# Kernel optimization log

Measured on AMD Instinct MI355X. Metric: run time of the kernel, lower is better.

## Reference

```python
import jax, jax.numpy as jnp
import numpy as np
import math

B = 16384; IN_DIM = 512; OUT_DIM = 256
D_MODEL = 512; N_HEADS = 8; E_LAYERS = 3; D_FF = 2048
FACTOR = 5; EPS = 1e-5
E_HEAD = D_MODEL // N_HEADS


def setup_inputs() -> dict:
    key = jax.random.key(0)
    ks = jax.random.split(key, 16)
    def w(k, shape):
        return jax.random.normal(k, shape, dtype=jnp.float32) * 0.02
    return {
        "x": jax.random.normal(ks[0], (B, IN_DIM), dtype=jnp.float32),
        "w_in": w(ks[1], (IN_DIM, D_MODEL)), "b_in": jnp.zeros((D_MODEL,), jnp.float32),
        "wq": w(ks[2], (D_MODEL, D_MODEL)), "bq": jnp.zeros((D_MODEL,), jnp.float32),
        "wk": w(ks[3], (D_MODEL, D_MODEL)), "bk": jnp.zeros((D_MODEL,), jnp.float32),
        "wv": w(ks[4], (D_MODEL, D_MODEL)), "bv": jnp.zeros((D_MODEL,), jnp.float32),
        "wo": w(ks[5], (D_MODEL, D_MODEL)), "bo": jnp.zeros((D_MODEL,), jnp.float32),
        "conv1_w": w(ks[6], (E_LAYERS, D_MODEL, D_FF)), "conv1_b": jnp.zeros((E_LAYERS, D_FF), jnp.float32),
        "conv2_w": w(ks[7], (E_LAYERS, D_FF, D_MODEL)), "conv2_b": jnp.zeros((E_LAYERS, D_MODEL), jnp.float32),
        "n1_g": jnp.ones((E_LAYERS, D_MODEL), jnp.float32), "n1_b": jnp.zeros((E_LAYERS, D_MODEL), jnp.float32),
        "n2_g": jnp.ones((E_LAYERS, D_MODEL), jnp.float32), "n2_b": jnp.zeros((E_LAYERS, D_MODEL), jnp.float32),
        "norm_g": jnp.ones((D_MODEL,), jnp.float32), "norm_b": jnp.zeros((D_MODEL,), jnp.float32),
        "w1": w(ks[8], (D_MODEL, D_FF)), "b1": jnp.zeros((D_FF,), jnp.float32),
        "w2": w(ks[9], (D_FF, OUT_DIM)), "b2": jnp.zeros((OUT_DIM,), jnp.float32),
    }


def _layernorm(x, g, b):
    m = jnp.mean(x, axis=-1, keepdims=True)
    v = jnp.mean(jnp.square(x - m), axis=-1, keepdims=True)
    return (x - m) * jax.lax.rsqrt(v + EPS) * g + b


def _prob_attention(q, k, v):
    # q,k,v: [B,H,L,E]; Informer ProbAttention with mask_flag=False.
    Bq, H, L, Eh = q.shape
    L_K = k.shape[2]
    # static (Python-level) sparse-attention sizes, as in the source
    U_part = min(L_K, max(1, FACTOR * int(np.ceil(np.log(max(L_K, 1.1))))))
    u = min(L, max(1, FACTOR * int(np.ceil(np.log(max(L, 1.1))))))
    step = L_K // max(1, U_part)
    idx = jnp.arange(0, L_K, step)                      # deterministic key sample
    k_s = k[:, :, idx, :]                               # [B,H,S,E] (no L_Q expand needed)
    qk_s = jnp.einsum('bhle,bhse->bhls', q, k_s)        # sampled QK scores
    M = qk_s.max(-1) - qk_s.sum(-1) / L_K               # sparsity measure [B,H,L]
    _, top = jax.lax.top_k(M, u)                        # top-u query indices [B,H,u]
    q_r = jnp.take_along_axis(q, top[..., None], axis=2)  # gather Q_reduce [B,H,u,E]
    scale = 1.0 / math.sqrt(Eh)
    scores = jnp.einsum('bhue,bhke->bhuk', q_r, k) * scale
    attn = jax.nn.softmax(scores, axis=-1)
    upd = jnp.einsum('bhuk,bhkd->bhud', attn, v)        # [B,H,u,D]
    # initial context = mean of V (mask_flag=False), then scatter top-u rows
    ctx = jnp.broadcast_to(v.mean(axis=2, keepdims=True), (Bq, H, L, v.shape[-1]))
    bi = jnp.arange(Bq)[:, None, None]
    hi = jnp.arange(H)[None, :, None]
    return ctx.at[bi, hi, top].set(upd)


def _attention_layer(x, wq, bq, wk, bk, wv, bv, wo, bo):
    Bx, L, _ = x.shape
    def proj(w, b):
        return (x @ w + b).reshape(Bx, L, N_HEADS, E_HEAD).transpose(0, 2, 1, 3)
    ctx = _prob_attention(proj(wq, bq), proj(wk, bk), proj(wv, bv))
    ctx = ctx.transpose(0, 2, 1, 3).reshape(Bx, L, -1)
    return ctx @ wo + bo


def _forward(x, w_in, b_in, wq, bq, wk, bk, wv, bv, wo, bo,
             conv1_w, conv1_b, conv2_w, conv2_b,
             n1_g, n1_b, n2_g, n2_b, norm_g, norm_b, w1, b1, w2, b2):
    h = (x @ w_in + b_in)[:, None, :]  # [B, 1, d_model] -- seq_len hardwired to 1
    for i in range(E_LAYERS):
        # NOTE: attention projection weights are SHARED across layers (as in source)
        a = _attention_layer(h, wq, bq, wk, bk, wv, bv, wo, bo)
        h = _layernorm(h + a, n1_g[i], n1_b[i])
        y = jax.nn.gelu(h @ conv1_w[i] + conv1_b[i], approximate=False)  # 1x1 conv == linear
        y = y @ conv2_w[i] + conv2_b[i]
        h = _layernorm(h + y, n2_g[i], n2_b[i])
    h = _layernorm(h, norm_g, norm_b)[:, 0, :]
    o = jax.nn.gelu(h @ w1 + b1, approximate=False)
    return o @ w2 + b2


def reference(x, w_in, b_in, wq, bq, wk, bk, wv, bv, wo, bo,
              conv1_w, conv1_b, conv2_w, conv2_b,
              n1_g, n1_b, n2_g, n2_b, norm_g, norm_b, w1, b1, w2, b2):
    return _forward(x, w_in, b_in, wq, bq, wk, bk, wv, bv, wo, bo,
                    conv1_w, conv1_b, conv2_w, conv2_b,
                    n1_g, n1_b, n2_g, n2_b, norm_g, norm_b, w1, b1, w2, b2)
```

## Files before the change

kernel.cpp:

```cpp
#include <hip/hip_runtime.h>
#include <hip/hip_bf16.h>
#include <math.h>

#define B_ROWS 16384
#define DM 512
#define DFF 2048
#define DOUT 256
#define EPSV 1e-5f

typedef __hip_bfloat16 bf16;
typedef __attribute__((ext_vector_type(8))) short short8;
typedef __attribute__((ext_vector_type(4))) float f32x4;

__device__ __forceinline__ float gelu_f(float x) {
    return 0.5f * x * (1.0f + erff(x * 0.70710678118654752f));
}

__device__ __forceinline__ void gload16(const void* g, void* l) {
    __builtin_amdgcn_global_load_lds((const __attribute__((address_space(1))) void*)g,
                                     (__attribute__((address_space(3))) void*)l, 16, 0, 0);
}

template<bool GELU, bool OUTF, bool OUTB>
__global__ __launch_bounds__(256, 2)
void gemm_kernel(const bf16* __restrict__ A, const bf16* __restrict__ BT,
                 const float* __restrict__ bias,
                 float* __restrict__ Cf, bf16* __restrict__ Cb,
                 int M, int N, int K)
{
    __shared__ __align__(16) bf16 lA[128 * 32];
    __shared__ __align__(16) bf16 lB[128 * 32];

    const int t    = threadIdx.x;
    const int lane = t & 63;
    const int w    = t >> 6;
    const int wr   = w >> 1, wc = w & 1;
    const int fr   = lane & 15, kg = lane >> 4;
    const long bm = (long)blockIdx.y * 128;
    const long bn = (long)blockIdx.x * 128;

    const int lr = t >> 2;
    const int lc = (t & 3) * 8;

    const bf16* Ag0 = A + (bm + lr) * (long)K + lc;
    const bf16* Ag1 = Ag0 + 64L * K;
    const bf16* Bg0 = BT + (bn + lr) * (long)K + lc;
    const bf16* Bg1 = Bg0 + 64L * K;

    bf16* lAd0 = lA + t * 8;
    bf16* lAd1 = lAd0 + 2048;
    bf16* lBd0 = lB + t * 8;
    bf16* lBd1 = lBd0 + 2048;

    f32x4 acc[4][4];
#pragma unroll
    for (int i = 0; i < 4; i++)
#pragma unroll
        for (int j = 0; j < 4; j++) acc[i][j] = (f32x4){0.f, 0.f, 0.f, 0.f};

    const int nk = K >> 5;
    for (int kt = 0; kt < nk; ++kt) {
        gload16(Ag0, lAd0);
        gload16(Ag1, lAd1);
        gload16(Bg0, lBd0);
        gload16(Bg1, lBd1);
        Ag0 += 32; Ag1 += 32; Bg0 += 32; Bg1 += 32;
        __syncthreads();

        short8 af[4], bv[4];
#pragma unroll
        for (int m = 0; m < 4; m++)
            af[m] = *(const short8*)(lA + (wr * 64 + m * 16 + fr) * 32 + kg * 8);
#pragma unroll
        for (int n = 0; n < 4; n++)
            bv[n] = *(const short8*)(lB + (wc * 64 + n * 16 + fr) * 32 + kg * 8);
#pragma unroll
        for (int m = 0; m < 4; m++)
#pragma unroll
            for (int n = 0; n < 4; n++)
                acc[m][n] = __builtin_amdgcn_mfma_f32_16x16x32_bf16(af[m], bv[n], acc[m][n], 0, 0, 0);
        __syncthreads();
    }

#pragma unroll
    for (int m = 0; m < 4; m++) {
        const long row0 = bm + wr * 64 + m * 16 + kg * 4;
#pragma unroll
        for (int n = 0; n < 4; n++) {
            const long col = bn + wc * 64 + n * 16 + fr;
            const float bias_v = bias ? bias[col] : 0.0f;
#pragma unroll
            for (int r = 0; r < 4; r++) {
                float v = acc[m][n][r] + bias_v;
                if (GELU) v = gelu_f(v);
                const long idx = (row0 + r) * (long)N + col;
                if (OUTF) Cf[idx] = v;
                if (OUTB) Cb[idx] = __float2bfloat16(v);
            }
        }
    }
}

__global__ __launch_bounds__(256)
void ln_kernel(const float* __restrict__ x, const float* __restrict__ add,
               const float* __restrict__ g, const float* __restrict__ bb,
               float* __restrict__ outf, bf16* __restrict__ outb)
{
    const int w    = threadIdx.x >> 6;
    const int lane = threadIdx.x & 63;
    const long row = (long)blockIdx.x * 4 + w;
    const int c0   = lane * 8;

    const float* xr = x + row * DM + c0;
    float4 a0 = *(const float4*)xr;
    float4 a1 = *(const float4*)(xr + 4);
    float v[8] = {a0.x, a0.y, a0.z, a0.w, a1.x, a1.y, a1.z, a1.w};
    if (add) {
        const float* ar = add + row * DM + c0;
        float4 d0 = *(const float4*)ar;
        float4 d1 = *(const float4*)(ar + 4);
        v[0] += d0.x; v[1] += d0.y; v[2] += d0.z; v[3] += d0.w;
        v[4] += d1.x; v[5] += d1.y; v[6] += d1.z; v[7] += d1.w;
    }
    float s = 0.f;
#pragma unroll
    for (int j = 0; j < 8; j++) s += v[j];
#pragma unroll
    for (int off = 32; off > 0; off >>= 1) s += __shfl_xor(s, off);
    const float mean = s * (1.0f / 512.0f);

    float q = 0.f;
#pragma unroll
    for (int j = 0; j < 8; j++) { v[j] -= mean; q += v[j] * v[j]; }
#pragma unroll
    for (int off = 32; off > 0; off >>= 1) q += __shfl_xor(q, off);
    const float rstd = rsqrtf(q * (1.0f / 512.0f) + EPSV);

    float4 g0 = *(const float4*)(g + c0);
    float4 g1 = *(const float4*)(g + c0 + 4);
    float4 b0 = *(const float4*)(bb + c0);
    float4 b1 = *(const float4*)(bb + c0 + 4);
    float y[8];
    y[0] = v[0] * rstd * g0.x + b0.x; y[1] = v[1] * rstd * g0.y + b0.y;
    y[2] = v[2] * rstd * g0.z + b0.z; y[3] = v[3] * rstd * g0.w + b0.w;
    y[4] = v[4] * rstd * g1.x + b1.x; y[5] = v[5] * rstd * g1.y + b1.y;
    y[6] = v[6] * rstd * g1.z + b1.z; y[7] = v[7] * rstd * g1.w + b1.w;

    if (outf) {
        float* orow = outf + row * DM + c0;
        *(float4*)orow       = make_float4(y[0], y[1], y[2], y[3]);
        *(float4*)(orow + 4) = make_float4(y[4], y[5], y[6], y[7]);
    }
    if (outb) {
        bf16 tmpb[8];
#pragma unroll
        for (int j = 0; j < 8; j++) tmpb[j] = __float2bfloat16(y[j]);
        *(uint4*)(outb + row * DM + c0) = *(const uint4*)tmpb;
    }
}

__global__ __launch_bounds__(256)
void transpose_bf16_kernel(const float* __restrict__ src, bf16* __restrict__ dst, int K, int N)
{
    __shared__ float tile[32][33];
    const long boff = (long)blockIdx.z * K * N;
    src += boff; dst += boff;
    const int n0 = blockIdx.x * 32, k0 = blockIdx.y * 32;
    const int tx = threadIdx.x & 31, ty = threadIdx.x >> 5;
#pragma unroll
    for (int j = 0; j < 32; j += 8)
        tile[ty + j][tx] = src[(long)(k0 + ty + j) * N + n0 + tx];
    __syncthreads();
#pragma unroll
    for (int j = 0; j < 32; j += 8)
        dst[(long)(n0 + ty + j) * K + k0 + tx] = __float2bfloat16(tile[tx][ty + j]);
}

__global__ __launch_bounds__(256)
void cvt_kernel(const float* __restrict__ src, bf16* __restrict__ dst, long n4)
{
    const long i = (long)blockIdx.x * 256 + threadIdx.x;
    if (i >= n4) return;
    const float4 vv = *(const float4*)(src + i * 4);
    bf16 t[4] = {__float2bfloat16(vv.x), __float2bfloat16(vv.y),
                 __float2bfloat16(vv.z), __float2bfloat16(vv.w)};
    *(uint2*)(dst + i * 4) = *(const uint2*)t;
}

__global__ __launch_bounds__(256)
void ba_kernel(const float* __restrict__ bv, const float* __restrict__ wo,
               const float* __restrict__ bo, float* __restrict__ ba)
{
    const int n = blockIdx.x * 256 + threadIdx.x;
    float s = bo[n];
    for (int j = 0; j < DM; j++) s += bv[j] * wo[(long)j * DM + n];
    ba[n] = s;
}

extern "C" void kernel_launch(void* const* d_in, const int* in_sizes, int n_in,
                              void* d_out, int out_size, void* d_ws, size_t ws_size,
                              hipStream_t stream)
{
    const float* x       = (const float*)d_in[0];
    const float* w_in    = (const float*)d_in[1];
    const float* b_in    = (const float*)d_in[2];
    const float* wv      = (const float*)d_in[7];
    const float* bv      = (const float*)d_in[8];
    const float* wo      = (const float*)d_in[9];
    const float* bo      = (const float*)d_in[10];
    const float* conv1_w = (const float*)d_in[11];
    const float* conv1_b = (const float*)d_in[12];
    const float* conv2_w = (const float*)d_in[13];
    const float* conv2_b = (const float*)d_in[14];
    const float* n1_g    = (const float*)d_in[15];
    const float* n1_b    = (const float*)d_in[16];
    const float* n2_g    = (const float*)d_in[17];
    const float* n2_b    = (const float*)d_in[18];
    const float* norm_g  = (const float*)d_in[19];
    const float* norm_b  = (const float*)d_in[20];
    const float* w1      = (const float*)d_in[21];
    const float* b1      = (const float*)d_in[22];
    const float* w2      = (const float*)d_in[23];
    const float* b2      = (const float*)d_in[24];
    float* out = (float*)d_out;

    char* ws = (char*)d_ws;
    size_t off = 0;
    auto alloc = [&](size_t bytes) {
        char* p = ws + off;
        off += (bytes + 255) & ~(size_t)255;
        return p;
    };
    bf16*  xbf  = (bf16*) alloc((size_t)B_ROWS * DM * 2);
    float* h    = (float*)alloc((size_t)B_ROWS * DM * 4);
    bf16*  hbf  = (bf16*) alloc((size_t)B_ROWS * DM * 2);
    float* tmp  = (float*)alloc((size_t)B_ROWS * DM * 4);
    bf16*  y1   = (bf16*) alloc((size_t)B_ROWS * DFF * 2);
    bf16*  winT = (bf16*) alloc((size_t)DM * DM * 2);
    bf16*  woT  = (bf16*) alloc((size_t)DM * DM * 2);
    bf16*  wvbf = (bf16*) alloc((size_t)DM * DM * 2);
    bf16*  WaT  = (bf16*) alloc((size_t)DM * DM * 2);
    float* ba   = (float*)alloc((size_t)DM * 4);
    bf16*  c1T  = (bf16*) alloc((size_t)3 * DFF * DM * 2);
    bf16*  c2T  = (bf16*) alloc((size_t)3 * DM * DFF * 2);
    bf16*  w1T  = (bf16*) alloc((size_t)DFF * DM * 2);
    bf16*  w2T  = (bf16*) alloc((size_t)DOUT * DFF * 2);

    dim3 blk(256);

    cvt_kernel<<<(B_ROWS * DM / 4 + 255) / 256, blk, 0, stream>>>(x, xbf, (long)B_ROWS * DM / 4);
    cvt_kernel<<<(DM * DM / 4 + 255) / 256, blk, 0, stream>>>(wv, wvbf, (long)DM * DM / 4);
    transpose_bf16_kernel<<<dim3(DM / 32, DM / 32, 1), blk, 0, stream>>>(w_in, winT, DM, DM);
    transpose_bf16_kernel<<<dim3(DM / 32, DM / 32, 1), blk, 0, stream>>>(wo, woT, DM, DM);
    transpose_bf16_kernel<<<dim3(DFF / 32, DM / 32, 3), blk, 0, stream>>>(conv1_w, c1T, DM, DFF);
    transpose_bf16_kernel<<<dim3(DM / 32, DFF / 32, 3), blk, 0, stream>>>(conv2_w, c2T, DFF, DM);
    transpose_bf16_kernel<<<dim3(DFF / 32, DM / 32, 1), blk, 0, stream>>>(w1, w1T, DM, DFF);
    transpose_bf16_kernel<<<dim3(DOUT / 32, DFF / 32, 1), blk, 0, stream>>>(w2, w2T, DFF, DOUT);
    ba_kernel<<<2, blk, 0, stream>>>(bv, wo, bo, ba);
    gemm_kernel<false, false, true><<<dim3(4, 4), blk, 0, stream>>>(
        woT, wvbf, nullptr, nullptr, WaT, DM, DM, DM);

    gemm_kernel<false, true, true><<<dim3(4, 128), blk, 0, stream>>>(
        xbf, winT, b_in, h, hbf, B_ROWS, DM, DM);

    for (int i = 0; i < 3; i++) {
        gemm_kernel<false, true, false><<<dim3(4, 128), blk, 0, stream>>>(
            hbf, WaT, ba, tmp, nullptr, B_ROWS, DM, DM);
        ln_kernel<<<B_ROWS / 4, blk, 0, stream>>>(h, tmp, n1_g + i * DM, n1_b + i * DM, h, hbf);
        gemm_kernel<true, false, true><<<dim3(16, 128), blk, 0, stream>>>(
            hbf, c1T + (size_t)i * DFF * DM, conv1_b + i * DFF, nullptr, y1, B_ROWS, DFF, DM);
        gemm_kernel<false, true, false><<<dim3(4, 128), blk, 0, stream>>>(
            y1, c2T + (size_t)i * DM * DFF, conv2_b + i * DM, tmp, nullptr, B_ROWS, DM, DFF);
        ln_kernel<<<B_ROWS / 4, blk, 0, stream>>>(h, tmp, n2_g + i * DM, n2_b + i * DM, h, hbf);
    }

    ln_kernel<<<B_ROWS / 4, blk, 0, stream>>>(h, nullptr, norm_g, norm_b, nullptr, hbf);
    gemm_kernel<true, false, true><<<dim3(16, 128), blk, 0, stream>>>(
        hbf, w1T, b1, nullptr, y1, B_ROWS, DFF, DM);
    gemm_kernel<false, true, false><<<dim3(2, 128), blk, 0, stream>>>(
        y1, w2T, b2, out, nullptr, B_ROWS, DOUT, DFF);
}
```

Before: 835.4 us.

## Fuse residual add and LayerNorm into N=512 GEMM epilogues, add XCD swizzle

Introduces a gemm_ln_kernel that computes full 512-wide rows per block (32 rows × 512 cols), adds bias and residual, then performs the LayerNorm in the epilogue via cross-wave LDS reduction, removing the separate ln_kernel launches and the fp32 tmp round-trip. The last layer's conv2 GEMM also fuses the final LayerNorm. A block-index swizzle across XCDs is added to the generic GEMM for L2 locality. Trade-offs: the fused kernel uses small M tiles (32 rows) with a single-buffered K loop and only 512 blocks, so MFMA efficiency and occupancy may drop, particularly for the K=2048 conv2 GEMM. Variance is computed as E[x²]-mean², which is less numerically stable than the two-pass form.

```diff
diff --git a/kernel.cpp b/kernel.cpp
--- a/kernel.cpp
+++ b/kernel.cpp
@@ -19,6 +19,11 @@
 __device__ __forceinline__ void gload16(const void* g, void* l) {
     __builtin_amdgcn_global_load_lds((const __attribute__((address_space(1))) void*)g,
                                      (__attribute__((address_space(3))) void*)l, 16, 0, 0);
+}
+
+__device__ __forceinline__ int xcd_swz(int bid, int nwg) {
+    const int cpx = nwg >> 3;
+    return (bid & 7) * cpx + (bid >> 3);
 }
 
 template<bool GELU, bool OUTF, bool OUTB>
@@ -36,8 +41,11 @@
     const int w    = t >> 6;
     const int wr   = w >> 1, wc = w & 1;
     const int fr   = lane & 15, kg = lane >> 4;
-    const long bm = (long)blockIdx.y * 128;
-    const long bn = (long)blockIdx.x * 128;
+
+    int bid = xcd_swz(blockIdx.y * gridDim.x + blockIdx.x, gridDim.x * gridDim.y);
+    const int bx = bid % gridDim.x, by = bid / gridDim.x;
+    const long bm = (long)by * 128;
+    const long bn = (long)bx * 128;
 
     const int lr = t >> 2;
     const int lc = (t & 3) * 8;
@@ -101,62 +109,195 @@
     }
 }
 
-__global__ __launch_bounds__(256)
-void ln_kernel(const float* __restrict__ x, const float* __restrict__ add,
-               const float* __restrict__ g, const float* __restrict__ bb,
-               float* __restrict__ outf, bf16* __restrict__ outb)
-{
-    const int w    = threadIdx.x >> 6;
-    const int lane = threadIdx.x & 63;
-    const long row = (long)blockIdx.x * 4 + w;
-    const int c0   = lane * 8;
-
-    const float* xr = x + row * DM + c0;
-    float4 a0 = *(const float4*)xr;
-    float4 a1 = *(const float4*)(xr + 4);
-    float v[8] = {a0.x, a0.y, a0.z, a0.w, a1.x, a1.y, a1.z, a1.w};
-    if (add) {
-        const float* ar = add + row * DM + c0;
-        float4 d0 = *(const float4*)ar;
-        float4 d1 = *(const float4*)(ar + 4);
-        v[0] += d0.x; v[1] += d0.y; v[2] += d0.z; v[3] += d0.w;
-        v[4] += d1.x; v[5] += d1.y; v[6] += d1.z; v[7] += d1.w;
-    }
-    float s = 0.f;
-#pragma unroll
-    for (int j = 0; j < 8; j++) s += v[j];
-#pragma unroll
-    for (int off = 32; off > 0; off >>= 1) s += __shfl_xor(s, off);
-    const float mean = s * (1.0f / 512.0f);
-
-    float q = 0.f;
-#pragma unroll
-    for (int j = 0; j < 8; j++) { v[j] -= mean; q += v[j] * v[j]; }
-#pragma unroll
-    for (int off = 32; off > 0; off >>= 1) q += __shfl_xor(q, off);
-    const float rstd = rsqrtf(q * (1.0f / 512.0f) + EPSV);
-
-    float4 g0 = *(const float4*)(g + c0);
-    float4 g1 = *(const float4*)(g + c0 + 4);
-    float4 b0 = *(const float4*)(bb + c0);
-    float4 b1 = *(const float4*)(bb + c0 + 4);
-    float y[8];
-    y[0] = v[0] * rstd * g0.x + b0.x; y[1] = v[1] * rstd * g0.y + b0.y;
-    y[2] = v[2] * rstd * g0.z + b0.z; y[3] = v[3] * rstd * g0.w + b0.w;
-    y[4] = v[4] * rstd * g1.x + b1.x; y[5] = v[5] * rstd * g1.y + b1.y;
-    y[6] = v[6] * rstd * g1.z + b1.z; y[7] = v[7] * rstd * g1.w + b1.w;
-
-    if (outf) {
-        float* orow = outf + row * DM + c0;
-        *(float4*)orow       = make_float4(y[0], y[1], y[2], y[3]);
-        *(float4*)(orow + 4) = make_float4(y[4], y[5], y[6], y[7]);
-    }
-    if (outb) {
-        bf16 tmpb[8];
-#pragma unroll
-        for (int j = 0; j < 8; j++) tmpb[j] = __float2bfloat16(y[j]);
-        *(uint4*)(outb + row * DM + c0) = *(const uint4*)tmpb;
-    }
+template<bool DOUBLE_LN, bool OUTF>
+__global__ __launch_bounds__(256, 2)
+void gemm_ln_kernel(const bf16* __restrict__ A, const bf16* __restrict__ BT,
+                    const float* __restrict__ bias, const float* __restrict__ resid,
+                    const float* __restrict__ g1, const float* __restrict__ b1,
+                    const float* __restrict__ g2, const float* __restrict__ b2,
+                    float* __restrict__ outf, bf16* __restrict__ outb,
+                    int M, int K)
+{
+    __shared__ __align__(16) bf16 lA[32 * 32];
+    __shared__ __align__(16) bf16 lB[512 * 32];
+
+    const int t    = threadIdx.x;
+    const int lane = t & 63;
+    const int w    = t >> 6;
+    const int fr   = lane & 15, kg = lane >> 4;
+
+    const int bid = xcd_swz(blockIdx.x, gridDim.x);
+    const long bm = (long)bid * 32;
+
+    const int lr = t >> 2;
+    const int lc = (t & 3) * 8;
+
+    const bf16* Ag = A + (bm + (lr & 31)) * (long)K + lc;
+    const bf16* Bg = BT + lr * (long)K + lc;
+
+    f32x4 acc[2][8];
+#pragma unroll
+    for (int m = 0; m < 2; m++)
+#pragma unroll
+        for (int n = 0; n < 8; n++) acc[m][n] = (f32x4){0.f, 0.f, 0.f, 0.f};
+
+    const int nk = K >> 5;
+    for (int kt = 0; kt < nk; ++kt) {
+        if (t < 128) gload16(Ag, lA + t * 8);
+#pragma unroll
+        for (int i = 0; i < 8; i++)
+            gload16(Bg + (size_t)(i * 64) * K, lB + i * 2048 + t * 8);
+        Ag += 32; Bg += 32;
+        __syncthreads();
+
+        short8 af[2], bv[8];
+#pragma unroll
+        for (int m = 0; m < 2; m++)
+            af[m] = *(const short8*)(lA + (m * 16 + fr) * 32 + kg * 8);
+#pragma unroll
+        for (int n = 0; n < 8; n++)
+            bv[n] = *(const short8*)(lB + (w * 128 + n * 16 + fr) * 32 + kg * 8);
+#pragma unroll
+        for (int m = 0; m < 2; m++)
+#pragma unroll
+            for (int n = 0; n < 8; n++)
+                acc[m][n] = __builtin_amdgcn_mfma_f32_16x16x32_bf16(af[m], bv[n], acc[m][n], 0, 0, 0);
+        __syncthreads();
+    }
+
+    float bias_v[8];
+#pragma unroll
+    for (int n = 0; n < 8; n++) bias_v[n] = bias[w * 128 + n * 16 + fr];
+
+#pragma unroll
+    for (int m = 0; m < 2; m++)
+#pragma unroll
+        for (int r = 0; r < 4; r++) {
+            const long row = bm + m * 16 + kg * 4 + r;
+            const float* rr = resid + row * DM + w * 128 + fr;
+#pragma unroll
+            for (int n = 0; n < 8; n++)
+                acc[m][n][r] += bias_v[n] + rr[n * 16];
+        }
+
+    float* red = (float*)lA;
+
+    float mean_[2][4], rstd_[2][4];
+    {
+        float S1[2][4], S2[2][4];
+#pragma unroll
+        for (int m = 0; m < 2; m++)
+#pragma unroll
+            for (int r = 0; r < 4; r++) {
+                float s1 = 0.f, s2 = 0.f;
+#pragma unroll
+                for (int n = 0; n < 8; n++) { float v = acc[m][n][r]; s1 += v; s2 += v * v; }
+#pragma unroll
+                for (int mk = 1; mk <= 8; mk <<= 1) { s1 += __shfl_xor(s1, mk); s2 += __shfl_xor(s2, mk); }
+                S1[m][r] = s1; S2[m][r] = s2;
+            }
+        if (fr == 0) {
+#pragma unroll
+            for (int m = 0; m < 2; m++)
+#pragma unroll
+                for (int r = 0; r < 4; r++) {
+                    const int rw = m * 16 + kg * 4 + r;
+                    red[w * 32 + rw] = S1[m][r];
+                    red[128 + w * 32 + rw] = S2[m][r];
+                }
+        }
+        __syncthreads();
+#pragma unroll
+        for (int m = 0; m < 2; m++)
+#pragma unroll
+            for (int r = 0; r < 4; r++) {
+                const int rw = m * 16 + kg * 4 + r;
+                const float s1 = red[rw] + red[32 + rw] + red[64 + rw] + red[96 + rw];
+                const float s2 = red[128 + rw] + red[160 + rw] + red[192 + rw] + red[224 + rw];
+                const float mu = s1 * (1.0f / 512.0f);
+                mean_[m][r] = mu;
+                rstd_[m][r] = rsqrtf(s2 * (1.0f / 512.0f) - mu * mu + EPSV);
+            }
+    }
+
+    {
+        float gv[8], bv1[8];
+#pragma unroll
+        for (int n = 0; n < 8; n++) {
+            gv[n]  = g1[w * 128 + n * 16 + fr];
+            bv1[n] = b1[w * 128 + n * 16 + fr];
+        }
+#pragma unroll
+        for (int m = 0; m < 2; m++)
+#pragma unroll
+            for (int r = 0; r < 4; r++) {
+                const float mu = mean_[m][r], rs = rstd_[m][r];
+#pragma unroll
+                for (int n = 0; n < 8; n++)
+                    acc[m][n][r] = (acc[m][n][r] - mu) * rs * gv[n] + bv1[n];
+            }
+    }
+
+    if (DOUBLE_LN) {
+        __syncthreads();
+        float S1[2][4], S2[2][4];
+#pragma unroll
+        for (int m = 0; m < 2; m++)
+#pragma unroll
+            for (int r = 0; r < 4; r++) {
+                float s1 = 0.f, s2 = 0.f;
+#pragma unroll
+                for (int n = 0; n < 8; n++) { float v = acc[m][n][r]; s1 += v; s2 += v * v; }
+#pragma unroll
+                for (int mk = 1; mk <= 8; mk <<= 1) { s1 += __shfl_xor(s1, mk); s2 += __shfl_xor(s2, mk); }
+                S1[m][r] = s1; S2[m][r] = s2;
+            }
+        if (fr == 0) {
+#pragma unroll
+            for (int m = 0; m < 2; m++)
+#pragma unroll
+                for (int r = 0; r < 4; r++) {
+                    const int rw = m * 16 + kg * 4 + r;
+                    red[w * 32 + rw] = S1[m][r];
+                    red[128 + w * 32 + rw] = S2[m][r];
+                }
+        }
+        __syncthreads();
+        float gv[8], bv2[8];
+#pragma unroll
+        for (int n = 0; n < 8; n++) {
+            gv[n]  = g2[w * 128 + n * 16 + fr];
+            bv2[n] = b2[w * 128 + n * 16 + fr];
+        }
+#pragma unroll
+        for (int m = 0; m < 2; m++)
+#pragma unroll
+            for (int r = 0; r < 4; r++) {
+                const int rw = m * 16 + kg * 4 + r;
+                const float s1 = red[rw] + red[32 + rw] + red[64 + rw] + red[96 + rw];
+                const float s2 = red[128 + rw] + red[160 + rw] + red[192 + rw] + red[224 + rw];
+                const float mu = s1 * (1.0f / 512.0f);
+                const float rs = rsqrtf(s2 * (1.0f / 512.0f) - mu * mu + EPSV);
+#pragma unroll
+                for (int n = 0; n < 8; n++)
+                    acc[m][n][r] = (acc[m][n][r] - mu) * rs * gv[n] + bv2[n];
+            }
+    }
+
+#pragma unroll
+    for (int m = 0; m < 2; m++)
+#pragma unroll
+        for (int r = 0; r < 4; r++) {
+            const long row = bm + m * 16 + kg * 4 + r;
+            float* of = OUTF ? (outf + row * DM + w * 128 + fr) : nullptr;
+            bf16* ob = outb + row * DM + w * 128 + fr;
+#pragma unroll
+            for (int n = 0; n < 8; n++) {
+                const float v = acc[m][n][r];
+                if (OUTF) of[n * 16] = v;
+                ob[n * 16] = __float2bfloat16(v);
+            }
+        }
 }
 
 __global__ __launch_bounds__(256)
@@ -234,7 +375,6 @@
     bf16*  xbf  = (bf16*) alloc((size_t)B_ROWS * DM * 2);
     float* h    = (float*)alloc((size_t)B_ROWS * DM * 4);
     bf16*  hbf  = (bf16*) alloc((size_t)B_ROWS * DM * 2);
-    float* tmp  = (float*)alloc((size_t)B_ROWS * DM * 4);
     bf16*  y1   = (bf16*) alloc((size_t)B_ROWS * DFF * 2);
     bf16*  winT = (bf16*) alloc((size_t)DM * DM * 2);
     bf16*  woT  = (bf16*) alloc((size_t)DM * DM * 2);
@@ -264,17 +404,24 @@
         xbf, winT, b_in, h, hbf, B_ROWS, DM, DM);
 
     for (int i = 0; i < 3; i++) {
-        gemm_kernel<false, true, false><<<dim3(4, 128), blk, 0, stream>>>(
-            hbf, WaT, ba, tmp, nullptr, B_ROWS, DM, DM);
-        ln_kernel<<<B_ROWS / 4, blk, 0, stream>>>(h, tmp, n1_g + i * DM, n1_b + i * DM, h, hbf);
+        gemm_ln_kernel<false, true><<<512, blk, 0, stream>>>(
+            hbf, WaT, ba, h, n1_g + i * DM, n1_b + i * DM, nullptr, nullptr,
+            h, hbf, B_ROWS, DM);
         gemm_kernel<true, false, true><<<dim3(16, 128), blk, 0, stream>>>(
             hbf, c1T + (size_t)i * DFF * DM, conv1_b + i * DFF, nullptr, y1, B_ROWS, DFF, DM);
-        gemm_kernel<false, true, false><<<dim3(4, 128), blk, 0, stream>>>(
-            y1, c2T + (size_t)i * DM * DFF, conv2_b + i * DM, tmp, nullptr, B_ROWS, DM, DFF);
-        ln_kernel<<<B_ROWS / 4, blk, 0, stream>>>(h, tmp, n2_g + i * DM, n2_b + i * DM, h, hbf);
-    }
-
-    ln_kernel<<<B_ROWS / 4, blk, 0, stream>>>(h, nullptr, norm_g, norm_b, nullptr, hbf);
+        if (i < 2) {
+            gemm_ln_kernel<false, true><<<512, blk, 0, stream>>>(
+                y1, c2T + (size_t)i * DM * DFF, conv2_b + i * DM, h,
+                n2_g + i * DM, n2_b + i * DM, nullptr, nullptr,
+                h, hbf, B_ROWS, DFF);
+        } else {
+            gemm_ln_kernel<true, false><<<512, blk, 0, stream>>>(
+                y1, c2T + (size_t)i * DM * DFF, conv2_b + i * DM, h,
+                n2_g + i * DM, n2_b + i * DM, norm_g, norm_b,
+                nullptr, hbf, B_ROWS, DFF);
+        }
+    }
+
     gemm_kernel<true, false, true><<<dim3(16, 128), blk, 0, stream>>>(
         hbf, w1T, b1, nullptr, y1, B_ROWS, DFF, DM);
     gemm_kernel<false, true, false><<<dim3(2, 128), blk, 0, stream>>>(
```

Result: no change. 828.3 us (-0.8%).

## Double-buffer GEMM LDS tiles, swizzle blocks across XCDs, store residuals in bf16

Applied to the files above, without the earlier changes.

The GEMM kernel now double-buffers its LDS tiles. It issues the next k-tile's global-to-LDS loads before computing on the current tile, which lets each iteration use a single barrier. Block indices are remapped so neighbouring tiles land on the same XCD, which should improve L2 reuse. The attention and FFN outputs that feed layernorm are written as bf16 instead of fp32, halving that intermediate traffic at some cost in precision. LDS use doubles, which may reduce occupancy.

```diff
diff --git a/kernel.cpp b/kernel.cpp
--- a/kernel.cpp
+++ b/kernel.cpp
@@ -16,9 +16,18 @@
     return 0.5f * x * (1.0f + erff(x * 0.70710678118654752f));
 }
 
+__device__ __forceinline__ float bf2f(short s) {
+    return __uint_as_float(((unsigned int)(unsigned short)s) << 16);
+}
+
 __device__ __forceinline__ void gload16(const void* g, void* l) {
     __builtin_amdgcn_global_load_lds((const __attribute__((address_space(1))) void*)g,
                                      (__attribute__((address_space(3))) void*)l, 16, 0, 0);
+}
+
+__device__ __forceinline__ int xcd_swz(int bid, int nwg) {
+    const int cpx = nwg >> 3;
+    return (bid & 7) * cpx + (bid >> 3);
 }
 
 template<bool GELU, bool OUTF, bool OUTB>
@@ -28,16 +37,19 @@
                  float* __restrict__ Cf, bf16* __restrict__ Cb,
                  int M, int N, int K)
 {
-    __shared__ __align__(16) bf16 lA[128 * 32];
-    __shared__ __align__(16) bf16 lB[128 * 32];
+    __shared__ __align__(16) bf16 lA[2][128 * 32];
+    __shared__ __align__(16) bf16 lB[2][128 * 32];
 
     const int t    = threadIdx.x;
     const int lane = t & 63;
     const int w    = t >> 6;
     const int wr   = w >> 1, wc = w & 1;
     const int fr   = lane & 15, kg = lane >> 4;
-    const long bm = (long)blockIdx.y * 128;
-    const long bn = (long)blockIdx.x * 128;
+
+    int bid = xcd_swz(blockIdx.y * gridDim.x + blockIdx.x, gridDim.x * gridDim.y);
+    const int bx = bid % gridDim.x, by = bid / gridDim.x;
+    const long bm = (long)by * 128;
+    const long bn = (long)bx * 128;
 
     const int lr = t >> 2;
     const int lc = (t & 3) * 8;
@@ -47,11 +59,6 @@
     const bf16* Bg0 = BT + (bn + lr) * (long)K + lc;
     const bf16* Bg1 = Bg0 + 64L * K;
 
-    bf16* lAd0 = lA + t * 8;
-    bf16* lAd1 = lAd0 + 2048;
-    bf16* lBd0 = lB + t * 8;
-    bf16* lBd1 = lBd0 + 2048;
-
     f32x4 acc[4][4];
 #pragma unroll
     for (int i = 0; i < 4; i++)
@@ -59,27 +66,40 @@
         for (int j = 0; j < 4; j++) acc[i][j] = (f32x4){0.f, 0.f, 0.f, 0.f};
 
     const int nk = K >> 5;
+
+    gload16(Ag0, &lA[0][t * 8]);
+    gload16(Ag1, &lA[0][2048 + t * 8]);
+    gload16(Bg0, &lB[0][t * 8]);
+    gload16(Bg1, &lB[0][2048 + t * 8]);
+    Ag0 += 32; Ag1 += 32; Bg0 += 32; Bg1 += 32;
+    __syncthreads();
+
+    int cur = 0;
     for (int kt = 0; kt < nk; ++kt) {
-        gload16(Ag0, lAd0);
-        gload16(Ag1, lAd1);
-        gload16(Bg0, lBd0);
-        gload16(Bg1, lBd1);
-        Ag0 += 32; Ag1 += 32; Bg0 += 32; Bg1 += 32;
-        __syncthreads();
+        if (kt + 1 < nk) {
+            const int nxt = cur ^ 1;
+            gload16(Ag0, &lA[nxt][t * 8]);
+            gload16(Ag1, &lA[nxt][2048 + t * 8]);
+            gload16(Bg0, &lB[nxt][t * 8]);
+            gload16(Bg1, &lB[nxt][2048 + t * 8]);
+            Ag0 += 32; Ag1 += 32; Bg0 += 32; Bg1 += 32;
+        }
 
         short8 af[4], bv[4];
 #pragma unroll
         for (int m = 0; m < 4; m++)
-            af[m] = *(const short8*)(lA + (wr * 64 + m * 16 + fr) * 32 + kg * 8);
+            af[m] = *(const short8*)(&lA[cur][(wr * 64 + m * 16 + fr) * 32 + kg * 8]);
 #pragma unroll
         for (int n = 0; n < 4; n++)
-            bv[n] = *(const short8*)(lB + (wc * 64 + n * 16 + fr) * 32 + kg * 8);
+            bv[n] = *(const short8*)(&lB[cur][(wc * 64 + n * 16 + fr) * 32 + kg * 8]);
 #pragma unroll
         for (int m = 0; m < 4; m++)
 #pragma unroll
             for (int n = 0; n < 4; n++)
                 acc[m][n] = __builtin_amdgcn_mfma_f32_16x16x32_bf16(af[m], bv[n], acc[m][n], 0, 0, 0);
+
         __syncthreads();
+        cur ^= 1;
     }
 
 #pragma unroll
@@ -101,8 +121,9 @@
     }
 }
 
+template<bool HASADD, bool OUTF>
 __global__ __launch_bounds__(256)
-void ln_kernel(const float* __restrict__ x, const float* __restrict__ add,
+void ln_kernel(const float* __restrict__ x, const bf16* __restrict__ add,
                const float* __restrict__ g, const float* __restrict__ bb,
                float* __restrict__ outf, bf16* __restrict__ outb)
 {
@@ -115,12 +136,10 @@
     float4 a0 = *(const float4*)xr;
     float4 a1 = *(const float4*)(xr + 4);
     float v[8] = {a0.x, a0.y, a0.z, a0.w, a1.x, a1.y, a1.z, a1.w};
-    if (add) {
-        const float* ar = add + row * DM + c0;
-        float4 d0 = *(const float4*)ar;
-        float4 d1 = *(const float4*)(ar + 4);
-        v[0] += d0.x; v[1] += d0.y; v[2] += d0.z; v[3] += d0.w;
-        v[4] += d1.x; v[5] += d1.y; v[6] += d1.z; v[7] += d1.w;
+    if (HASADD) {
+        short8 ad = *(const short8*)(add + row * DM + c0);
+#pragma unroll
+        for (int j = 0; j < 8; j++) v[j] += bf2f(ad[j]);
     }
     float s = 0.f;
 #pragma unroll
@@ -146,12 +165,12 @@
     y[4] = v[4] * rstd * g1.x + b1.x; y[5] = v[5] * rstd * g1.y + b1.y;
     y[6] = v[6] * rstd * g1.z + b1.z; y[7] = v[7] * rstd * g1.w + b1.w;
 
-    if (outf) {
+    if (OUTF) {
         float* orow = outf + row * DM + c0;
         *(float4*)orow       = make_float4(y[0], y[1], y[2], y[3]);
         *(float4*)(orow + 4) = make_float4(y[4], y[5], y[6], y[7]);
     }
-    if (outb) {
+    {
         bf16 tmpb[8];
 #pragma unroll
         for (int j = 0; j < 8; j++) tmpb[j] = __float2bfloat16(y[j]);
@@ -234,7 +253,7 @@
     bf16*  xbf  = (bf16*) alloc((size_t)B_ROWS * DM * 2);
     float* h    = (float*)alloc((size_t)B_ROWS * DM * 4);
     bf16*  hbf  = (bf16*) alloc((size_t)B_ROWS * DM * 2);
-    float* tmp  = (float*)alloc((size_t)B_ROWS * DM * 4);
+    bf16*  tmpb = (bf16*) alloc((size_t)B_ROWS * DM * 2);
     bf16*  y1   = (bf16*) alloc((size_t)B_ROWS * DFF * 2);
     bf16*  winT = (bf16*) alloc((size_t)DM * DM * 2);
     bf16*  woT  = (bf16*) alloc((size_t)DM * DM * 2);
@@ -264,17 +283,20 @@
         xbf, winT, b_in, h, hbf, B_ROWS, DM, DM);
 
     for (int i = 0; i < 3; i++) {
-        gemm_kernel<false, true, false><<<dim3(4, 128), blk, 0, stream>>>(
-            hbf, WaT, ba, tmp, nullptr, B_ROWS, DM, DM);
-        ln_kernel<<<B_ROWS / 4, blk, 0, stream>>>(h, tmp, n1_g + i * DM, n1_b + i * DM, h, hbf);
+        gemm_kernel<false, false, true><<<dim3(4, 128), blk, 0, stream>>>(
+            hbf, WaT, ba, nullptr, tmpb, B_ROWS, DM, DM);
+        ln_kernel<true, true><<<B_ROWS / 4, blk, 0, stream>>>(
+            h, tmpb, n1_g + i * DM, n1_b + i * DM, h, hbf);
         gemm_kernel<true, false, true><<<dim3(16, 128), blk, 0, stream>>>(
             hbf, c1T + (size_t)i * DFF * DM, conv1_b + i * DFF, nullptr, y1, B_ROWS, DFF, DM);
-        gemm_kernel<false, true, false><<<dim3(4, 128), blk, 0, stream>>>(
-            y1, c2T + (size_t)i * DM * DFF, conv2_b + i * DM, tmp, nullptr, B_ROWS, DM, DFF);
-        ln_kernel<<<B_ROWS / 4, blk, 0, stream>>>(h, tmp, n2_g + i * DM, n2_b + i * DM, h, hbf);
-    }
-
-    ln_kernel<<<B_ROWS / 4, blk, 0, stream>>>(h, nullptr, norm_g, norm_b, nullptr, hbf);
+        gemm_kernel<false, false, true><<<dim3(4, 128), blk, 0, stream>>>(
+            y1, c2T + (size_t)i * DM * DFF, conv2_b + i * DM, nullptr, tmpb, B_ROWS, DM, DFF);
+        ln_kernel<true, true><<<B_ROWS / 4, blk, 0, stream>>>(
+            h, tmpb, n2_g + i * DM, n2_b + i * DM, h, hbf);
+    }
+
+    ln_kernel<false, false><<<B_ROWS / 4, blk, 0, stream>>>(
+        h, nullptr, norm_g, norm_b, nullptr, hbf);
     gemm_kernel<true, false, true><<<dim3(16, 128), blk, 0, stream>>>(
         hbf, w1T, b1, nullptr, y1, B_ROWS, DFF, DM);
     gemm_kernel<false, true, false><<<dim3(2, 128), blk, 0, stream>>>(
```

After: 789.3 us. 5.5% less time.
